# Kernel tuning notes

Hardware: AMD Instinct MI355X
Metric: run time of the kernel (lower is better)

The kernel has to match this reference:

```python
import jax, jax.numpy as jnp
import numpy as np

NUM_EMBEDDINGS = 512
EMBEDDING_DIM = 64
COMMITMENT_COST = 0.25


def setup_inputs() -> dict:
    key = jax.random.key(0)
    k1, k2 = jax.random.split(key)
    inputs = jax.random.normal(k1, (8, 64, 32, 32, 32), dtype=jnp.float32)
    bound = 1.0 / NUM_EMBEDDINGS
    codebook = jax.random.uniform(
        k2, (NUM_EMBEDDINGS, EMBEDDING_DIM), dtype=jnp.float32,
        minval=-bound, maxval=bound)
    return {"inputs": inputs, "codebook": codebook}


def reference(inputs, codebook):
    # [B, C, D, H, W] -> [B, D, H, W, C]
    x = jnp.transpose(inputs, (0, 2, 3, 4, 1))
    input_shape = x.shape
    flat = x.reshape(-1, EMBEDDING_DIM)  # [N, C]

    # squared L2 distances to codebook: [N, K]
    distances = (
        jnp.sum(flat ** 2, axis=1, keepdims=True)
        + jnp.sum(codebook ** 2, axis=1)
        - 2.0 * flat @ codebook.T
    )
    encoding_indices = jnp.argmin(distances, axis=1)  # [N]
    quantized = codebook[encoding_indices].reshape(input_shape)

    sg = jax.lax.stop_gradient
    vq_loss = (
        jnp.mean((sg(quantized) - x) ** 2)
        + COMMITMENT_COST * jnp.mean((quantized - sg(x)) ** 2)
    )

    # straight-through estimator
    quantized_for_decoder = x + sg(quantized - x)
    # [B, D, H, W, C] -> [B, C, D, H, W]
    quantized_for_decoder = jnp.transpose(quantized_for_decoder, (0, 4, 1, 2, 3))
    return quantized_for_decoder, vq_loss, encoding_indices
```

## Files before the change

kernel.cpp:

```cpp
#include <hip/hip_runtime.h>

#define CC 64
#define NN 262144
#define NELEM 16777216
#define KK 512
#define CHUNK 128
#define NCHUNK 4
#define ROWS 128
#define TAU 4e-5f
#define CAP 28672

#define WS_CNT  0
#define WS_PART 64
#define WS_B    16448
#define WS_E1   18496
#define WS_E2   84032
#define WS_LIST 149568

typedef short short8 __attribute__((ext_vector_type(8)));
typedef float f32x4 __attribute__((ext_vector_type(4)));

__device__ __forceinline__ unsigned short bf16_rne(float x) {
    unsigned u = __float_as_uint(x);
    unsigned r = u + 0x7FFFu + ((u >> 16) & 1u);
    return (unsigned short)(r >> 16);
}
__device__ __forceinline__ float bf16_back(unsigned short h) {
    return __uint_as_float(((unsigned)h) << 16);
}

__global__ __launch_bounds__(256) void vq_prep(
    const float* __restrict__ cb, unsigned char* __restrict__ ws)
{
#pragma clang fp contract(off)
    const int k = blockIdx.x * 256 + threadIdx.x;
    if (k == 0) *(unsigned*)(ws + WS_CNT) = 0u;

    float e[CC];
    const float4* ep = (const float4*)(cb + k * CC);
    #pragma unroll
    for (int i = 0; i < 16; ++i) {
        float4 v = ep[i];
        e[4*i] = v.x; e[4*i+1] = v.y; e[4*i+2] = v.z; e[4*i+3] = v.w;
    }
    float q[8];
    #pragma unroll
    for (int j = 0; j < 8; ++j) q[j] = e[j] * e[j];
    #pragma unroll
    for (int i = 1; i < 8; ++i) {
        #pragma unroll
        for (int j = 0; j < 8; ++j) { float sq = e[8*i+j] * e[8*i+j]; q[j] = q[j] + sq; }
    }
    ((float*)(ws + WS_B))[k] = ((q[0]+q[1])+(q[2]+q[3]))+((q[4]+q[5])+(q[6]+q[7]));

    char* e1 = (char*)(ws + WS_E1);
    char* e2 = (char*)(ws + WS_E2);
    #pragma unroll
    for (int s = 0; s < 8; ++s) {
        short8 hi, lo;
        #pragma unroll
        for (int j = 0; j < 8; ++j) {
            float v = -2.0f * e[s*8 + j];
            unsigned short h = bf16_rne(v);
            hi[j] = (short)h;
            lo[j] = (short)bf16_rne(v - bf16_back(h));
        }
        const int off = k * 128 + ((s * 16) ^ ((k & 7) << 4));
        *(short8*)(e1 + off) = hi;
        *(short8*)(e2 + off) = lo;
    }
}

__global__ __launch_bounds__(256, 4) void vq_mfma(
    const float* __restrict__ in, const float* __restrict__ cb,
    unsigned char* __restrict__ ws,
    float* __restrict__ out_q, float* __restrict__ out_idx)
{
#pragma clang fp contract(off)
    __shared__ short  e1s[CHUNK * CC];
    __shared__ short  e2s[CHUNK * CC];
    __shared__ float  Bl_s[KK];
    __shared__ float  Al[ROWS];
    __shared__ int    idx_s[ROWS];
    __shared__ double red_s[256];

    const int tid  = threadIdx.x;
    const int lane = tid & 63;
    const int w    = tid >> 6;
    const int nb   = blockIdx.x * ROWS;
    const int bblk = nb >> 15;
    const float* xbase = in + ((size_t)bblk << 21) + (nb & 32767);

    if (tid < ROWS) {
        const float* xa = xbase + tid;
        float r[8];
        #pragma unroll
        for (int j = 0; j < 8; ++j) { float v = xa[(size_t)j << 15]; r[j] = v * v; }
        #pragma unroll
        for (int i = 1; i < 8; ++i) {
            #pragma unroll
            for (int j = 0; j < 8; ++j) {
                float v = xa[(size_t)(8*i + j) << 15];
                float sq = v * v;
                r[j] = r[j] + sq;
            }
        }
        Al[tid] = ((r[0]+r[1])+(r[2]+r[3]))+((r[4]+r[5])+(r[6]+r[7]));
    }
    {
        const float* wsB = (const float*)(ws + WS_B);
        Bl_s[tid] = wsB[tid]; Bl_s[tid + 256] = wsB[tid + 256];
    }
    __syncthreads();

    short8 a1[2][2], a2[2][2];
    {
        const int c0 = (lane >> 4) * 8;
        #pragma unroll
        for (int rt = 0; rt < 2; ++rt) {
            const float* xp = xbase + (w*32 + rt*16 + (lane & 15));
            #pragma unroll
            for (int j = 0; j < 8; ++j) {
                float v0 = xp[(size_t)(c0 + j) << 15];
                float v1 = xp[(size_t)(c0 + j + 32) << 15];
                unsigned short h0 = bf16_rne(v0), h1 = bf16_rne(v1);
                a1[rt][0][j] = (short)h0;
                a1[rt][1][j] = (short)h1;
                a2[rt][0][j] = (short)bf16_rne(v0 - bf16_back(h0));
                a2[rt][1][j] = (short)bf16_rne(v1 - bf16_back(h1));
            }
        }
    }

    float s1v[2][4], s2v[2][4];
    #pragma unroll
    for (int rt = 0; rt < 2; ++rt)
        #pragma unroll
        for (int r = 0; r < 4; ++r) { s1v[rt][r] = 3.4e38f; s2v[rt][r] = 3.4e38f; }

    const unsigned lanec = (unsigned)(lane & 15);

    for (int ch = 0; ch < NCHUNK; ++ch) {
        __syncthreads();
        {
            const char* s1p = (const char*)(ws + WS_E1 + ch * 16384) + tid * 16;
            const char* s2p = (const char*)(ws + WS_E2 + ch * 16384) + tid * 16;
            char* d1p = (char*)e1s + tid * 16;
            char* d2p = (char*)e2s + tid * 16;
            #pragma unroll
            for (int i = 0; i < 4; ++i) {
                __builtin_amdgcn_global_load_lds(
                    (const __attribute__((address_space(1))) unsigned int*)(s1p + i*4096),
                    (__attribute__((address_space(3))) unsigned int*)(d1p + i*4096), 16, 0, 0);
                __builtin_amdgcn_global_load_lds(
                    (const __attribute__((address_space(1))) unsigned int*)(s2p + i*4096),
                    (__attribute__((address_space(3))) unsigned int*)(d2p + i*4096), 16, 0, 0);
            }
        }
        __syncthreads();

        #pragma unroll
        for (int t16 = 0; t16 < 8; ++t16) {
            const int kt = ch*8 + t16;
            const int codeL = t16*16 + (lane & 15);
            const unsigned pc = ((unsigned)kt << 4) | lanec;
            short8 b1[2], b2[2];
            #pragma unroll
            for (int h = 0; h < 2; ++h) {
                const int byteoff = codeL*128 + (((4*h + (lane>>4)) * 16) ^ ((codeL & 7) << 4));
                b1[h] = *(const short8*)((const char*)e1s + byteoff);
                b2[h] = *(const short8*)((const char*)e2s + byteoff);
            }
            const float Bs = Bl_s[ch*CHUNK + codeL];
            #pragma unroll
            for (int rt = 0; rt < 2; ++rt) {
                f32x4 acc = {Bs, Bs, Bs, Bs};
                acc = __builtin_amdgcn_mfma_f32_16x16x32_bf16(a1[rt][0], b1[0], acc, 0, 0, 0);
                acc = __builtin_amdgcn_mfma_f32_16x16x32_bf16(a1[rt][1], b1[1], acc, 0, 0, 0);
                acc = __builtin_amdgcn_mfma_f32_16x16x32_bf16(a2[rt][0], b1[0], acc, 0, 0, 0);
                acc = __builtin_amdgcn_mfma_f32_16x16x32_bf16(a2[rt][1], b1[1], acc, 0, 0, 0);
                acc = __builtin_amdgcn_mfma_f32_16x16x32_bf16(a1[rt][0], b2[0], acc, 0, 0, 0);
                acc = __builtin_amdgcn_mfma_f32_16x16x32_bf16(a1[rt][1], b2[1], acc, 0, 0, 0);
                #pragma unroll
                for (int r = 0; r < 4; ++r) {
                    float dp = __uint_as_float((__float_as_uint(acc[r]) & 0xFFFFFE00u) | pc);
                    s2v[rt][r] = __builtin_amdgcn_fmed3f(dp, s1v[rt][r], s2v[rt][r]);
                    s1v[rt][r] = __builtin_fminf(s1v[rt][r], dp);
                }
            }
        }
    }

    unsigned* cnt  = (unsigned*)(ws + WS_CNT);
    unsigned* list = (unsigned*)(ws + WS_LIST);
    double lsum = 0.0;
    #pragma unroll
    for (int rt = 0; rt < 2; ++rt) {
        #pragma unroll
        for (int r = 0; r < 4; ++r) {
            float s1 = s1v[rt][r], s2 = s2v[rt][r];
            #pragma unroll
            for (int off = 1; off < 16; off <<= 1) {
                float s1o = __shfl_xor(s1, off);
                float s2o = __shfl_xor(s2, off);
                s2 = __builtin_fminf(__builtin_fminf(s2, s2o), __builtin_fmaxf(s1, s1o));
                s1 = __builtin_fminf(s1, s1o);
            }
            if ((lane & 15) == 0) {
                const int rl = w*32 + rt*16 + (lane>>4)*4 + r;
                const int code = (int)(__float_as_uint(s1) & 511u);
                out_idx[nb + rl] = (float)code;
                idx_s[rl] = code;
                if (s2 - s1 < TAU) {
                    unsigned pos = atomicAdd(cnt, 1u);
                    if (pos < CAP) list[pos] = (unsigned)(nb + rl);
                }
                lsum += (double)(Al[rl] + s1);
            }
        }
    }
    red_s[tid] = lsum;
    __syncthreads();

    {
        const int row = tid >> 1, c0 = (tid & 1) << 5;
        const int myidx = idx_s[row];
        const float4* cbr = (const float4*)cb + myidx*16 + (c0 >> 2);
        float* qp = out_q + ((size_t)bblk << 21) + (nb & 32767) + row;
        #pragma unroll
        for (int cg = 0; cg < 8; ++cg) {
            float4 ev = cbr[cg];
            qp[(size_t)(c0 + 4*cg + 0) << 15] = ev.x;
            qp[(size_t)(c0 + 4*cg + 1) << 15] = ev.y;
            qp[(size_t)(c0 + 4*cg + 2) << 15] = ev.z;
            qp[(size_t)(c0 + 4*cg + 3) << 15] = ev.w;
        }
    }
    for (int off = 128; off; off >>= 1) {
        if (tid < off) red_s[tid] += red_s[tid + off];
        __syncthreads();
    }
    if (tid == 0) ((double*)(ws + WS_PART))[blockIdx.x] = red_s[0];
}

__global__ __launch_bounds__(256, 2) void vq_recheck(
    const float* __restrict__ in, const float* __restrict__ cb,
    unsigned char* __restrict__ ws,
    float* __restrict__ out_q, float* __restrict__ out_loss,
    float* __restrict__ out_idx)
{
#pragma clang fp contract(off)
    __shared__ float xs[4][CC];
    const int tid  = threadIdx.x;
    const int lane = tid & 63;
    const int w    = tid >> 6;

    if (blockIdx.x == 0 && w == 0) {
        const double* partials = (const double*)(ws + WS_PART);
        double p = 0.0;
        #pragma unroll
        for (int j = 0; j < 32; ++j) p += partials[lane*32 + j];
        #pragma unroll
        for (int off = 1; off < 64; off <<= 1) p += __shfl_xor(p, off);
        if (lane == 0) *out_loss = (float)(1.25 * p / (double)NELEM);
    }

    const unsigned m = *(const unsigned*)(ws + WS_CNT);
    const unsigned* list = (const unsigned*)(ws + WS_LIST);
    const float* Bw = (const float*)(ws + WS_B);
    const unsigned total = (m <= CAP) ? m : NN;

    for (unsigned i = blockIdx.x * 4 + w; i < total; i += gridDim.x * 4) {
        const unsigned n = (m <= CAP) ? list[i] : i;
        const int oldidx = (int)out_idx[n];
        const float* xp = in + ((size_t)(n >> 15) << 21) + (n & 32767);

        xs[w][lane] = xp[(size_t)lane << 15];

        float r0[8];
        #pragma unroll
        for (int j = 0; j < 8; ++j) { float v = xs[w][j]; r0[j] = v * v; }
        #pragma unroll
        for (int ii = 1; ii < 8; ++ii) {
            #pragma unroll
            for (int j = 0; j < 8; ++j) { float v = xs[w][8*ii + j]; float sq = v * v; r0[j] = r0[j] + sq; }
        }
        const float A = ((r0[0]+r0[1])+(r0[2]+r0[3]))+((r0[4]+r0[5])+(r0[6]+r0[7]));

        float cacc[8];
        #pragma unroll
        for (int jj = 0; jj < 8; ++jj) cacc[jj] = 0.f;
        const float4* cb4 = (const float4*)cb;
        #pragma unroll 1
        for (int c4 = 0; c4 < 16; ++c4) {
            float4 x4 = *(const float4*)&xs[w][c4 * 4];
            #pragma unroll
            for (int jj = 0; jj < 8; ++jj) {
                float4 ev = cb4[(size_t)(jj*64 + lane) * 16 + c4];
                cacc[jj] = __builtin_fmaf(x4.x, ev.x, cacc[jj]);
                cacc[jj] = __builtin_fmaf(x4.y, ev.y, cacc[jj]);
                cacc[jj] = __builtin_fmaf(x4.z, ev.z, cacc[jj]);
                cacc[jj] = __builtin_fmaf(x4.w, ev.w, cacc[jj]);
            }
        }

        float best = 3.4e38f; int bk = 0;
        #pragma unroll
        for (int jj = 0; jj < 8; ++jj) {
            const int k = jj*64 + lane;
            const float t1 = A + Bw[k];
            const float t2 = 2.0f * cacc[jj];
            const float D = t1 - t2;
            if (D < best) { best = D; bk = k; }
        }
        #pragma unroll
        for (int off = 1; off < 64; off <<= 1) {
            float bo = __shfl_xor(best, off);
            int   ko = __shfl_xor(bk, off);
            if (bo < best || (bo == best && ko < bk)) { best = bo; bk = ko; }
        }
        if (bk != oldidx) {
            if (lane == 0) out_idx[n] = (float)bk;
            out_q[((size_t)(n >> 15) << 21) + ((size_t)lane << 15) + (n & 32767)] = cb[bk*CC + lane];
        }
    }
}

extern "C" void kernel_launch(void* const* d_in, const int* in_sizes, int n_in,
                              void* d_out, int out_size, void* d_ws, size_t ws_size,
                              hipStream_t stream) {
    const float* in = (const float*)d_in[0];
    const float* cb = (const float*)d_in[1];
    float* out      = (float*)d_out;
    float* out_q    = out;
    float* out_loss = out + NELEM;
    float* out_idx  = out + NELEM + 1;
    unsigned char* ws = (unsigned char*)d_ws;

    vq_prep<<<2, 256, 0, stream>>>(cb, ws);
    vq_mfma<<<NN / ROWS, 256, 0, stream>>>(in, cb, ws, out_q, out_idx);
    vq_recheck<<<1024, 256, 0, stream>>>(in, cb, ws, out_q, out_loss, out_idx);
}
```

Measured before the change: 111.5 us.

## Fuse near-tie recheck and loss reduction into main MFMA kernel

```diff
diff --git a/kernel.cpp b/kernel.cpp
--- a/kernel.cpp
+++ b/kernel.cpp
@@ -7,15 +7,14 @@
 #define CHUNK 128
 #define NCHUNK 4
 #define ROWS 128
+#define NBLK (NN/ROWS)
 #define TAU 4e-5f
-#define CAP 28672
-
-#define WS_CNT  0
-#define WS_PART 64
-#define WS_B    16448
-#define WS_E1   18496
-#define WS_E2   84032
-#define WS_LIST 149568
+
+#define WS_TICKET 0
+#define WS_LACC   8
+#define WS_B      64
+#define WS_E1     2112
+#define WS_E2     67648
 
 typedef short short8 __attribute__((ext_vector_type(8)));
 typedef float f32x4 __attribute__((ext_vector_type(4)));
@@ -34,7 +33,10 @@
 {
 #pragma clang fp contract(off)
     const int k = blockIdx.x * 256 + threadIdx.x;
-    if (k == 0) *(unsigned*)(ws + WS_CNT) = 0u;
+    if (k == 0) {
+        *(unsigned*)(ws + WS_TICKET) = 0u;
+        *(double*)(ws + WS_LACC) = 0.0;
+    }
 
     float e[CC];
     const float4* ep = (const float4*)(cb + k * CC);
@@ -74,15 +76,18 @@
 __global__ __launch_bounds__(256, 4) void vq_mfma(
     const float* __restrict__ in, const float* __restrict__ cb,
     unsigned char* __restrict__ ws,
-    float* __restrict__ out_q, float* __restrict__ out_idx)
+    float* __restrict__ out_q, float* __restrict__ out_loss,
+    float* __restrict__ out_idx)
 {
 #pragma clang fp contract(off)
-    __shared__ short  e1s[CHUNK * CC];
-    __shared__ short  e2s[CHUNK * CC];
-    __shared__ float  Bl_s[KK];
-    __shared__ float  Al[ROWS];
-    __shared__ int    idx_s[ROWS];
-    __shared__ double red_s[256];
+    __shared__ short    e1s[CHUNK * CC];
+    __shared__ short    e2s[CHUNK * CC];
+    __shared__ float    Bl_s[KK];
+    __shared__ float    Al[ROWS];
+    __shared__ int      idx_s[ROWS];
+    __shared__ double   red_s[256];
+    __shared__ unsigned flag_s[ROWS];
+    __shared__ unsigned nflag_s;
 
     const int tid  = threadIdx.x;
     const int lane = tid & 63;
@@ -90,6 +95,8 @@
     const int nb   = blockIdx.x * ROWS;
     const int bblk = nb >> 15;
     const float* xbase = in + ((size_t)bblk << 21) + (nb & 32767);
+
+    if (tid == 0) nflag_s = 0u;
 
     if (tid < ROWS) {
         const float* xa = xbase + tid;
@@ -191,8 +198,6 @@
         }
     }
 
-    unsigned* cnt  = (unsigned*)(ws + WS_CNT);
-    unsigned* list = (unsigned*)(ws + WS_LIST);
     double lsum = 0.0;
     #pragma unroll
     for (int rt = 0; rt < 2; ++rt) {
@@ -212,8 +217,8 @@
                 out_idx[nb + rl] = (float)code;
                 idx_s[rl] = code;
                 if (s2 - s1 < TAU) {
-                    unsigned pos = atomicAdd(cnt, 1u);
-                    if (pos < CAP) list[pos] = (unsigned)(nb + rl);
+                    unsigned p = atomicAdd(&nflag_s, 1u);
+                    flag_s[p] = (unsigned)rl;
                 }
                 lsum += (double)(Al[rl] + s1);
             }
@@ -240,89 +245,69 @@
         if (tid < off) red_s[tid] += red_s[tid + off];
         __syncthreads();
     }
-    if (tid == 0) ((double*)(ws + WS_PART))[blockIdx.x] = red_s[0];
-}
-
-__global__ __launch_bounds__(256, 2) void vq_recheck(
-    const float* __restrict__ in, const float* __restrict__ cb,
-    unsigned char* __restrict__ ws,
-    float* __restrict__ out_q, float* __restrict__ out_loss,
-    float* __restrict__ out_idx)
-{
-#pragma clang fp contract(off)
-    __shared__ float xs[4][CC];
-    const int tid  = threadIdx.x;
-    const int lane = tid & 63;
-    const int w    = tid >> 6;
-
-    if (blockIdx.x == 0 && w == 0) {
-        const double* partials = (const double*)(ws + WS_PART);
-        double p = 0.0;
-        #pragma unroll
-        for (int j = 0; j < 32; ++j) p += partials[lane*32 + j];
-        #pragma unroll
-        for (int off = 1; off < 64; off <<= 1) p += __shfl_xor(p, off);
-        if (lane == 0) *out_loss = (float)(1.25 * p / (double)NELEM);
-    }
-
-    const unsigned m = *(const unsigned*)(ws + WS_CNT);
-    const unsigned* list = (const unsigned*)(ws + WS_LIST);
-    const float* Bw = (const float*)(ws + WS_B);
-    const unsigned total = (m <= CAP) ? m : NN;
-
-    for (unsigned i = blockIdx.x * 4 + w; i < total; i += gridDim.x * 4) {
-        const unsigned n = (m <= CAP) ? list[i] : i;
-        const int oldidx = (int)out_idx[n];
-        const float* xp = in + ((size_t)(n >> 15) << 21) + (n & 32767);
-
-        xs[w][lane] = xp[(size_t)lane << 15];
-
-        float r0[8];
-        #pragma unroll
-        for (int j = 0; j < 8; ++j) { float v = xs[w][j]; r0[j] = v * v; }
-        #pragma unroll
-        for (int ii = 1; ii < 8; ++ii) {
-            #pragma unroll
-            for (int j = 0; j < 8; ++j) { float v = xs[w][8*ii + j]; float sq = v * v; r0[j] = r0[j] + sq; }
-        }
-        const float A = ((r0[0]+r0[1])+(r0[2]+r0[3]))+((r0[4]+r0[5])+(r0[6]+r0[7]));
-
-        float cacc[8];
-        #pragma unroll
-        for (int jj = 0; jj < 8; ++jj) cacc[jj] = 0.f;
+
+    bool isLast = false;
+    if (tid == 0) {
+        atomicAdd((double*)(ws + WS_LACC), red_s[0]);
+        __threadfence();
+        unsigned t = atomicAdd((unsigned*)(ws + WS_TICKET), 1u);
+        isLast = (t == (unsigned)(NBLK - 1));
+    }
+    __syncthreads();
+
+    {
+        const unsigned nf = nflag_s;
+        float* xrow = (float*)red_s;
         const float4* cb4 = (const float4*)cb;
-        #pragma unroll 1
-        for (int c4 = 0; c4 < 16; ++c4) {
-            float4 x4 = *(const float4*)&xs[w][c4 * 4];
+        for (unsigned fi = (unsigned)w; fi < nf; fi += 4) {
+            const int rl = (int)flag_s[fi];
+            const int n = nb + rl;
+            const float* xp = xbase + rl;
+            xrow[w*CC + lane] = xp[(size_t)lane << 15];
+
+            const float A = Al[rl];
+            float cacc[8];
+            #pragma unroll
+            for (int jj = 0; jj < 8; ++jj) cacc[jj] = 0.f;
+            #pragma unroll 1
+            for (int c4 = 0; c4 < 16; ++c4) {
+                float4 x4 = *(const float4*)&xrow[w*CC + c4*4];
+                #pragma unroll
+                for (int jj = 0; jj < 8; ++jj) {
+                    float4 ev = cb4[(size_t)(jj*64 + lane) * 16 + c4];
+                    cacc[jj] = __builtin_fmaf(x4.x, ev.x, cacc[jj]);
+                    cacc[jj] = __builtin_fmaf(x4.y, ev.y, cacc[jj]);
+                    cacc[jj] = __builtin_fmaf(x4.z, ev.z, cacc[jj]);
+                    cacc[jj] = __builtin_fmaf(x4.w, ev.w, cacc[jj]);
+                }
+            }
+            float best = 3.4e38f; int bk = 0;
             #pragma unroll
             for (int jj = 0; jj < 8; ++jj) {
-                float4 ev = cb4[(size_t)(jj*64 + lane) * 16 + c4];
-                cacc[jj] = __builtin_fmaf(x4.x, ev.x, cacc[jj]);
-                cacc[jj] = __builtin_fmaf(x4.y, ev.y, cacc[jj]);
-                cacc[jj] = __builtin_fmaf(x4.z, ev.z, cacc[jj]);
-                cacc[jj] = __builtin_fmaf(x4.w, ev.w, cacc[jj]);
-            }
-        }
-
-        float best = 3.4e38f; int bk = 0;
-        #pragma unroll
-        for (int jj = 0; jj < 8; ++jj) {
-            const int k = jj*64 + lane;
-            const float t1 = A + Bw[k];
-            const float t2 = 2.0f * cacc[jj];
-            const float D = t1 - t2;
-            if (D < best) { best = D; bk = k; }
-        }
-        #pragma unroll
-        for (int off = 1; off < 64; off <<= 1) {
-            float bo = __shfl_xor(best, off);
-            int   ko = __shfl_xor(bk, off);
-            if (bo < best || (bo == best && ko < bk)) { best = bo; bk = ko; }
-        }
-        if (bk != oldidx) {
-            if (lane == 0) out_idx[n] = (float)bk;
-            out_q[((size_t)(n >> 15) << 21) + ((size_t)lane << 15) + (n & 32767)] = cb[bk*CC + lane];
-        }
+                const int k = jj*64 + lane;
+                const float t1 = A + Bl_s[k];
+                const float t2 = 2.0f * cacc[jj];
+                const float D = t1 - t2;
+                if (D < best) { best = D; bk = k; }
+            }
+            #pragma unroll
+            for (int off = 1; off < 64; off <<= 1) {
+                float bo = __shfl_xor(best, off);
+                int   ko = __shfl_xor(bk, off);
+                if (bo < best || (bo == best && ko < bk)) { best = bo; bk = ko; }
+            }
+            if (bk != idx_s[rl]) {
+                if (lane == 0) out_idx[n] = (float)bk;
+                out_q[((size_t)(n >> 15) << 21) + ((size_t)lane << 15) + (n & 32767)]
+                    = cb[bk*CC + lane];
+            }
+        }
+    }
+
+    if (isLast) {
+        __threadfence();
+        double v = atomicAdd((double*)(ws + WS_LACC), 0.0);
+        *out_loss = (float)(1.25 * v / (double)NELEM);
     }
 }
 
@@ -338,6 +323,5 @@
     unsigned char* ws = (unsigned char*)d_ws;
 
     vq_prep<<<2, 256, 0, stream>>>(cb, ws);
-    vq_mfma<<<NN / ROWS, 256, 0, stream>>>(in, cb, ws, out_q, out_idx);
-    vq_recheck<<<1024, 256, 0, stream>>>(in, cb, ws, out_q, out_loss, out_idx);
-}
+    vq_mfma<<<NBLK, 256, 0, stream>>>(in, cb, ws, out_q, out_loss, out_idx);
+}
```

Result: slower. 231.6 us (+107.8%).
